# Kernel tuning notes

Measured on AMD Instinct MI355X. Metric: run time of the kernel, lower is better.

## Reference

```python
import jax, jax.numpy as jnp
import numpy as np

NUM_EXPERTS = 8
HIDDEN = 1024
FFN = 2048
TOKENS = 2048


def setup_inputs() -> dict:
    key = jax.random.key(0)
    k_x, k_idx, k_w1, k_w2 = jax.random.split(key, 4)
    scale = 0.02
    x = jax.random.normal(k_x, (TOKENS, HIDDEN), dtype=jnp.float32)
    expert_indices = jax.random.randint(k_idx, (TOKENS,), 0, NUM_EXPERTS, dtype=jnp.int64)
    W1 = jax.random.normal(k_w1, (NUM_EXPERTS, HIDDEN, FFN), dtype=jnp.float32) * scale
    b1 = jnp.zeros((NUM_EXPERTS, FFN), dtype=jnp.float32)
    W2 = jax.random.normal(k_w2, (NUM_EXPERTS, FFN, HIDDEN), dtype=jnp.float32) * scale
    b2 = jnp.zeros((NUM_EXPERTS, HIDDEN), dtype=jnp.float32)
    return {"x": x, "expert_indices": expert_indices, "W1": W1, "b1": b1, "W2": W2, "b2": b2}


def reference(x, expert_indices, W1, b1, W2, b2):
    # Each token routed to one expert's MLP: Linear -> GELU(exact) -> Linear.
    # Dropout is identity in eval mode. Loop is over the small fixed expert set.
    out = jnp.zeros_like(x)
    for e in range(NUM_EXPERTS):
        h = jax.nn.gelu(x @ W1[e] + b1[e], approximate=False)  # [T, FFN]
        y = h @ W2[e] + b2[e]                                   # [T, H]
        mask = (expert_indices == e)[:, None]
        out = out + jnp.where(mask, y, 0.0)
    return out
```

## Files before the change

kernel.cpp:

```cpp
#include <hip/hip_runtime.h>

#define T_TOK 2048
#define HID   1024
#define FFN   2048
#define NEXP  8
#define MAX_SLOTS 40

typedef __attribute__((ext_vector_type(8))) short bf16x8;
typedef __attribute__((ext_vector_type(4))) float f32x4;

__device__ __forceinline__ short f2bf(float f) {
    unsigned u = __builtin_bit_cast(unsigned, f);
    u = (u + 0x7fffu + ((u >> 16) & 1u)) >> 16;
    return (short)u;
}

__device__ __forceinline__ float gelu_exact(float x) {
    return 0.5f * x * (1.0f + erff(x * 0.70710678118654752f));
}

__device__ __forceinline__ void async_cp16(const short* g, short* l) {
    __builtin_amdgcn_global_load_lds(
        (const __attribute__((address_space(1))) unsigned int*)g,
        (__attribute__((address_space(3))) unsigned int*)l, 16, 0, 0);
}

__device__ __forceinline__ void wtrans_body(
        const float* __restrict__ W, short* __restrict__ WT,
        int K, int N, int e, int kblk, int nblk) {
    int tid = threadIdx.x;
    int w = tid >> 6, l = tid & 63;
    int kb = kblk * 32 + w * 8;
    int n4 = nblk * 256 + l * 4;
    const float* src = W + (size_t)e * K * N + (size_t)kb * N + n4;
    float4 v[8];
#pragma unroll
    for (int r = 0; r < 8; r++)
        v[r] = *(const float4*)(src + (size_t)r * N);
    int kpanel = kb >> 6;
    int kc = (kb >> 3) & 7;
    int npanel = n4 >> 7;
    int n_in = n4 & 127;
    int kpanels = K >> 6;
    short* dst = WT + (size_t)e * K * N
               + ((size_t)npanel * kpanels + kpanel) * 8192
               + kc * 1024 + n_in * 8;
#pragma unroll
    for (int j = 0; j < 4; j++) {
        bf16x8 o = {f2bf(((const float*)&v[0])[j]), f2bf(((const float*)&v[1])[j]),
                    f2bf(((const float*)&v[2])[j]), f2bf(((const float*)&v[3])[j]),
                    f2bf(((const float*)&v[4])[j]), f2bf(((const float*)&v[5])[j]),
                    f2bf(((const float*)&v[6])[j]), f2bf(((const float*)&v[7])[j])};
        *(bf16x8*)(dst + j * 8) = o;
    }
}

__global__ __launch_bounds__(256) void wtrans_w1_kernel(
        const float* __restrict__ W1, short* __restrict__ W1T) {
    int e = blockIdx.x >> 8, rem = blockIdx.x & 255;
    wtrans_body(W1, W1T, HID, FFN, e, rem & 31, rem >> 5);
}

__global__ __launch_bounds__(256) void wtrans_w2_kernel(
        const float* __restrict__ W2, short* __restrict__ W2T) {
    int e = blockIdx.x >> 8, rem = blockIdx.x & 255;
    wtrans_body(W2, W2T, FFN, HID, e, rem & 63, rem >> 6);
}

__global__ __launch_bounds__(256) void misc_kernel(
        const float* __restrict__ x, const int* __restrict__ idx,
        const float* __restrict__ b2,
        short* __restrict__ xb, float* __restrict__ out,
        int* __restrict__ offs, int* __restrict__ cnts,
        int* __restrict__ tokl,
        int* __restrict__ slot_e, int* __restrict__ slot_t0) {
    int bx = blockIdx.x;
    int tid = threadIdx.x;
    if (bx < 1024) {
        int i = (bx * 256 + tid) * 8;
        float4 v0 = *(const float4*)(x + i);
        float4 v1 = *(const float4*)(x + i + 4);
        bf16x8 r = {f2bf(v0.x), f2bf(v0.y), f2bf(v0.z), f2bf(v0.w),
                    f2bf(v1.x), f2bf(v1.y), f2bf(v1.z), f2bf(v1.w)};
        *(bf16x8*)(xb + i) = r;
    } else if (bx < 3072) {
        int t = bx - 1024;
        int e = idx[t];
        ((float4*)(out + (size_t)t * HID))[tid] =
            ((const float4*)(b2 + (size_t)e * HID))[tid];
    } else {
        __shared__ int c[NEXP], cur[NEXP], o[NEXP];
        if (tid < NEXP) { c[tid] = 0; cur[tid] = 0; }
        __syncthreads();
        for (int t = tid; t < T_TOK; t += 256) atomicAdd(&c[idx[t]], 1);
        __syncthreads();
        if (tid == 0) {
            int s = 0;
            for (int e = 0; e < NEXP; e++) { o[e] = s; s += c[e]; }
            int ns = 0;
            for (int e = 0; e < NEXP; e++)
                for (int t0 = 0; t0 < c[e]; t0 += 64) {
                    slot_e[ns] = e; slot_t0[ns] = t0; ns++;
                }
            for (; ns < MAX_SLOTS; ns++) slot_e[ns] = -1;
        }
        __syncthreads();
        if (tid < NEXP) { offs[tid] = o[tid]; cnts[tid] = c[tid]; }
        for (int t = tid; t < T_TOK; t += 256) {
            int e = idx[t];
            int p = o[e] + atomicAdd(&cur[e], 1);
            tokl[p] = t;
        }
    }
}

__global__ __launch_bounds__(256) void gemm1_kernel(
        const short* __restrict__ xb, const short* __restrict__ W1T,
        const float* __restrict__ b1,
        const int* __restrict__ offs, const int* __restrict__ cnts,
        const int* __restrict__ tokl,
        const int* __restrict__ slot_e, const int* __restrict__ slot_t0,
        short* __restrict__ hg) {
    int s = blockIdx.y;
    int e = slot_e[s];
    if (e < 0) return;
    int t0 = slot_t0[s], count = cnts[e], off = offs[e];
    int n0 = blockIdx.x * 128;

    __shared__ short As[64 * 64];
    __shared__ short Bs[8 * 128 * 8];
    __shared__ int stok[64];

    int tid = threadIdx.x;
    if (tid < 64) {
        int p = t0 + tid;
        stok[tid] = tokl[off + (p < count ? p : count - 1)];
    }
    __syncthreads();

    int w = tid >> 6, l = tid & 63, l15 = l & 15, quad = l >> 4;
    int wm = (w >> 1) * 32, wn = (w & 1) * 64;

    int m0 = w * 16 + (l >> 3), m1 = m0 + 8;
    int cs = l & 7;
    int c0 = (cs - m0) & 7, c1 = (cs - m1) & 7;
    const short* gA0 = xb + (size_t)stok[m0] * HID + c0 * 8;
    const short* gA1 = xb + (size_t)stok[m1] * HID + c1 * 8;
    short* lA0 = As + w * 1024 + l * 8;
    short* lA1 = lA0 + 512;

    const short* Bpan = W1T + (size_t)e * (FFN * HID)
                      + (size_t)(n0 >> 7) * ((HID >> 6) * 8192);
    int bo0 = (2 * w) * 1024 + l * 8;
    int bo1 = bo0 + 1024;
    int bo2 = bo0 + 512;
    int bo3 = bo1 + 512;

    f32x4 acc[2][4];
#pragma unroll
    for (int i = 0; i < 2; i++)
#pragma unroll
        for (int j = 0; j < 4; j++) acc[i][j] = (f32x4){0.f, 0.f, 0.f, 0.f};

    for (int kt = 0; kt < HID / 64; kt++) {
        const short* bp = Bpan + kt * 8192;
        async_cp16(gA0, lA0);
        async_cp16(gA1, lA1);
        async_cp16(bp + bo0, Bs + bo0);
        async_cp16(bp + bo1, Bs + bo1);
        async_cp16(bp + bo2, Bs + bo2);
        async_cp16(bp + bo3, Bs + bo3);
        gA0 += 64; gA1 += 64;
        __syncthreads();
        bf16x8 a[2][2], b[2][4];
#pragma unroll
        for (int kk = 0; kk < 2; kk++) {
#pragma unroll
            for (int mt = 0; mt < 2; mt++) {
                int m = wm + mt * 16 + l15;
                a[kk][mt] = *(const bf16x8*)&As[m * 64 + (((kk * 4 + quad) + m) & 7) * 8];
            }
#pragma unroll
            for (int nt = 0; nt < 4; nt++) {
                int n = wn + nt * 16 + l15;
                b[kk][nt] = *(const bf16x8*)&Bs[(kk * 4 + quad) * 1024 + n * 8];
            }
        }
#pragma unroll
        for (int kk = 0; kk < 2; kk++)
#pragma unroll
            for (int mt = 0; mt < 2; mt++)
#pragma unroll
                for (int nt = 0; nt < 4; nt++)
                    acc[mt][nt] = __builtin_amdgcn_mfma_f32_16x16x32_bf16(
                        a[kk][mt], b[kk][nt], acc[mt][nt], 0, 0, 0);
        __syncthreads();
    }

    const float* b1e = b1 + e * FFN + n0;
#pragma unroll
    for (int mt = 0; mt < 2; mt++) {
        int rbase = wm + mt * 16 + quad * 4;
#pragma unroll
        for (int nt = 0; nt < 4; nt++) {
            int coln = wn + nt * 16 + l15;
            float bb = b1e[coln];
#pragma unroll
            for (int r = 0; r < 4; r++) {
                int p = t0 + rbase + r;
                if (p < count)
                    hg[(size_t)(off + p) * FFN + n0 + coln] =
                        f2bf(gelu_exact(acc[mt][nt][r] + bb));
            }
        }
    }
}

__global__ __launch_bounds__(256) void gemm2_kernel(
        const short* __restrict__ hg, const short* __restrict__ W2T,
        const int* __restrict__ offs, const int* __restrict__ cnts,
        const int* __restrict__ tokl,
        const int* __restrict__ slot_e, const int* __restrict__ slot_t0,
        float* __restrict__ out) {
    int s = blockIdx.y;
    int e = slot_e[s];
    if (e < 0) return;
    int t0 = slot_t0[s], count = cnts[e], off = offs[e];
    int ks = blockIdx.z;
    int n0 = blockIdx.x * 128;

    __shared__ short As[64 * 64];
    __shared__ short Bs[8 * 128 * 8];

    int tid = threadIdx.x;
    int w = tid >> 6, l = tid & 63, l15 = l & 15, quad = l >> 4;
    int wm = (w >> 1) * 32, wn = (w & 1) * 64;

    int m0 = w * 16 + (l >> 3), m1 = m0 + 8;
    int cs = l & 7;
    int c0 = (cs - m0) & 7, c1 = (cs - m1) & 7;
    int g0 = off + (t0 + m0 < count ? t0 + m0 : count - 1);
    int g1 = off + (t0 + m1 < count ? t0 + m1 : count - 1);
    const short* gA0 = hg + (size_t)g0 * FFN + ks * 1024 + c0 * 8;
    const short* gA1 = hg + (size_t)g1 * FFN + ks * 1024 + c1 * 8;
    short* lA0 = As + w * 1024 + l * 8;
    short* lA1 = lA0 + 512;

    const short* Bpan = W2T + (size_t)e * (FFN * HID)
                      + (size_t)(n0 >> 7) * ((FFN >> 6) * 8192)
                      + (size_t)ks * 16 * 8192;
    int bo0 = (2 * w) * 1024 + l * 8;
    int bo1 = bo0 + 1024;
    int bo2 = bo0 + 512;
    int bo3 = bo1 + 512;

    f32x4 acc[2][4];
#pragma unroll
    for (int i = 0; i < 2; i++)
#pragma unroll
        for (int j = 0; j < 4; j++) acc[i][j] = (f32x4){0.f, 0.f, 0.f, 0.f};

    for (int kt = 0; kt < 16; kt++) {
        const short* bp = Bpan + kt * 8192;
        async_cp16(gA0, lA0);
        async_cp16(gA1, lA1);
        async_cp16(bp + bo0, Bs + bo0);
        async_cp16(bp + bo1, Bs + bo1);
        async_cp16(bp + bo2, Bs + bo2);
        async_cp16(bp + bo3, Bs + bo3);
        gA0 += 64; gA1 += 64;
        __syncthreads();
        bf16x8 a[2][2], b[2][4];
#pragma unroll
        for (int kk = 0; kk < 2; kk++) {
#pragma unroll
            for (int mt = 0; mt < 2; mt++) {
                int m = wm + mt * 16 + l15;
                a[kk][mt] = *(const bf16x8*)&As[m * 64 + (((kk * 4 + quad) + m) & 7) * 8];
            }
#pragma unroll
            for (int nt = 0; nt < 4; nt++) {
                int n = wn + nt * 16 + l15;
                b[kk][nt] = *(const bf16x8*)&Bs[(kk * 4 + quad) * 1024 + n * 8];
            }
        }
#pragma unroll
        for (int kk = 0; kk < 2; kk++)
#pragma unroll
            for (int mt = 0; mt < 2; mt++)
#pragma unroll
                for (int nt = 0; nt < 4; nt++)
                    acc[mt][nt] = __builtin_amdgcn_mfma_f32_16x16x32_bf16(
                        a[kk][mt], b[kk][nt], acc[mt][nt], 0, 0, 0);
        __syncthreads();
    }

#pragma unroll
    for (int mt = 0; mt < 2; mt++) {
        int rbase = wm + mt * 16 + quad * 4;
#pragma unroll
        for (int nt = 0; nt < 4; nt++) {
            int coln = n0 + wn + nt * 16 + l15;
#pragma unroll
            for (int r = 0; r < 4; r++) {
                int p = t0 + rbase + r;
                if (p < count) {
                    int tok = tokl[off + p];
                    atomicAdd(out + (size_t)tok * HID + coln, acc[mt][nt][r]);
                }
            }
        }
    }
}

extern "C" void kernel_launch(void* const* d_in, const int* in_sizes, int n_in,
                              void* d_out, int out_size, void* d_ws, size_t ws_size,
                              hipStream_t stream) {
    const float* x   = (const float*)d_in[0];
    const int*   idx = (const int*)d_in[1];
    const float* W1  = (const float*)d_in[2];
    const float* b1  = (const float*)d_in[3];
    const float* W2  = (const float*)d_in[4];
    const float* b2  = (const float*)d_in[5];
    float* out = (float*)d_out;

    const size_t META = 32768;
    int*   offs    = (int*)d_ws;
    int*   cnts    = offs + 8;
    int*   tokl    = offs + 16;
    int*   slot_e  = offs + 16 + T_TOK;
    int*   slot_t0 = slot_e + MAX_SLOTS;
    char*  base    = (char*)d_ws + META;
    short* xb  = (short*)base;
    short* hg  = (short*)(base + (size_t)T_TOK * HID * 2);
    short* W1T = (short*)(base + (size_t)T_TOK * HID * 2 + (size_t)T_TOK * FFN * 2);
    short* W2T = W1T + (size_t)NEXP * FFN * HID;

    wtrans_w1_kernel<<<2048, 256, 0, stream>>>(W1, W1T);
    wtrans_w2_kernel<<<2048, 256, 0, stream>>>(W2, W2T);
    misc_kernel<<<3073, 256, 0, stream>>>(
        x, idx, b2, xb, out, offs, cnts, tokl, slot_e, slot_t0);

    gemm1_kernel<<<dim3(FFN / 128, MAX_SLOTS), 256, 0, stream>>>(
        xb, W1T, b1, offs, cnts, tokl, slot_e, slot_t0, hg);
    gemm2_kernel<<<dim3(HID / 128, MAX_SLOTS, 2), 256, 0, stream>>>(
        hg, W2T, offs, cnts, tokl, slot_e, slot_t0, out);
}
```

Measured before the change: 236.3 us.

## Triple-buffer LDS tiles with async prefetch in both expert GEMM kernels

```diff
diff --git a/kernel.cpp b/kernel.cpp
--- a/kernel.cpp
+++ b/kernel.cpp
@@ -127,8 +127,8 @@
     int t0 = slot_t0[s], count = cnts[e], off = offs[e];
     int n0 = blockIdx.x * 128;
 
-    __shared__ short As[64 * 64];
-    __shared__ short Bs[8 * 128 * 8];
+    __shared__ short As[3 * 64 * 64];
+    __shared__ short Bs[3 * 8 * 128 * 8];
     __shared__ int stok[64];
 
     int tid = threadIdx.x;
@@ -146,8 +146,7 @@
     int c0 = (cs - m0) & 7, c1 = (cs - m1) & 7;
     const short* gA0 = xb + (size_t)stok[m0] * HID + c0 * 8;
     const short* gA1 = xb + (size_t)stok[m1] * HID + c1 * 8;
-    short* lA0 = As + w * 1024 + l * 8;
-    short* lA1 = lA0 + 512;
+    int aoff = w * 1024 + l * 8;
 
     const short* Bpan = W1T + (size_t)e * (FFN * HID)
                       + (size_t)(n0 >> 7) * ((HID >> 6) * 8192);
@@ -156,34 +155,48 @@
     int bo2 = bo0 + 512;
     int bo3 = bo1 + 512;
 
+    auto stage = [&](int buf, int kt) {
+        const short* bp = Bpan + (size_t)kt * 8192;
+        short* As_b = As + buf * 4096;
+        short* Bs_b = Bs + buf * 8192;
+        async_cp16(gA0 + kt * 64, As_b + aoff);
+        async_cp16(gA1 + kt * 64, As_b + aoff + 512);
+        async_cp16(bp + bo0, Bs_b + bo0);
+        async_cp16(bp + bo1, Bs_b + bo1);
+        async_cp16(bp + bo2, Bs_b + bo2);
+        async_cp16(bp + bo3, Bs_b + bo3);
+    };
+
     f32x4 acc[2][4];
 #pragma unroll
     for (int i = 0; i < 2; i++)
 #pragma unroll
         for (int j = 0; j < 4; j++) acc[i][j] = (f32x4){0.f, 0.f, 0.f, 0.f};
 
-    for (int kt = 0; kt < HID / 64; kt++) {
-        const short* bp = Bpan + kt * 8192;
-        async_cp16(gA0, lA0);
-        async_cp16(gA1, lA1);
-        async_cp16(bp + bo0, Bs + bo0);
-        async_cp16(bp + bo1, Bs + bo1);
-        async_cp16(bp + bo2, Bs + bo2);
-        async_cp16(bp + bo3, Bs + bo3);
-        gA0 += 64; gA1 += 64;
-        __syncthreads();
+    const int KT = HID / 64;
+    stage(0, 0); stage(1, 1); stage(2, 2);
+
+    int buf = 0;
+    for (int kt = 0; kt < KT; kt++) {
+        if (kt + 2 < KT)      asm volatile("s_waitcnt vmcnt(12)" ::: "memory");
+        else if (kt + 1 < KT) asm volatile("s_waitcnt vmcnt(6)" ::: "memory");
+        else                  asm volatile("s_waitcnt vmcnt(0)" ::: "memory");
+        __builtin_amdgcn_s_barrier();
+
+        const short* As_b = As + buf * 4096;
+        const short* Bs_b = Bs + buf * 8192;
         bf16x8 a[2][2], b[2][4];
 #pragma unroll
         for (int kk = 0; kk < 2; kk++) {
 #pragma unroll
             for (int mt = 0; mt < 2; mt++) {
                 int m = wm + mt * 16 + l15;
-                a[kk][mt] = *(const bf16x8*)&As[m * 64 + (((kk * 4 + quad) + m) & 7) * 8];
+                a[kk][mt] = *(const bf16x8*)&As_b[m * 64 + (((kk * 4 + quad) + m) & 7) * 8];
             }
 #pragma unroll
             for (int nt = 0; nt < 4; nt++) {
                 int n = wn + nt * 16 + l15;
-                b[kk][nt] = *(const bf16x8*)&Bs[(kk * 4 + quad) * 1024 + n * 8];
+                b[kk][nt] = *(const bf16x8*)&Bs_b[(kk * 4 + quad) * 1024 + n * 8];
             }
         }
 #pragma unroll
@@ -194,7 +207,11 @@
                 for (int nt = 0; nt < 4; nt++)
                     acc[mt][nt] = __builtin_amdgcn_mfma_f32_16x16x32_bf16(
                         a[kk][mt], b[kk][nt], acc[mt][nt], 0, 0, 0);
-        __syncthreads();
+
+        __builtin_amdgcn_sched_barrier(0);
+        __builtin_amdgcn_s_barrier();
+        if (kt + 3 < KT) stage(buf, kt + 3);
+        buf = buf + 1; if (buf == 3) buf = 0;
     }
 
     const float* b1e = b1 + e * FFN + n0;
@@ -229,8 +246,8 @@
     int ks = blockIdx.z;
     int n0 = blockIdx.x * 128;
 
-    __shared__ short As[64 * 64];
-    __shared__ short Bs[8 * 128 * 8];
+    __shared__ short As[3 * 64 * 64];
+    __shared__ short Bs[3 * 8 * 128 * 8];
 
     int tid = threadIdx.x;
     int w = tid >> 6, l = tid & 63, l15 = l & 15, quad = l >> 4;
@@ -243,8 +260,7 @@
     int g1 = off + (t0 + m1 < count ? t0 + m1 : count - 1);
     const short* gA0 = hg + (size_t)g0 * FFN + ks * 1024 + c0 * 8;
     const short* gA1 = hg + (size_t)g1 * FFN + ks * 1024 + c1 * 8;
-    short* lA0 = As + w * 1024 + l * 8;
-    short* lA1 = lA0 + 512;
+    int aoff = w * 1024 + l * 8;
 
     const short* Bpan = W2T + (size_t)e * (FFN * HID)
                       + (size_t)(n0 >> 7) * ((FFN >> 6) * 8192)
@@ -254,34 +270,48 @@
     int bo2 = bo0 + 512;
     int bo3 = bo1 + 512;
 
+    auto stage = [&](int buf, int kt) {
+        const short* bp = Bpan + (size_t)kt * 8192;
+        short* As_b = As + buf * 4096;
+        short* Bs_b = Bs + buf * 8192;
+        async_cp16(gA0 + kt * 64, As_b + aoff);
+        async_cp16(gA1 + kt * 64, As_b + aoff + 512);
+        async_cp16(bp + bo0, Bs_b + bo0);
+        async_cp16(bp + bo1, Bs_b + bo1);
+        async_cp16(bp + bo2, Bs_b + bo2);
+        async_cp16(bp + bo3, Bs_b + bo3);
+    };
+
     f32x4 acc[2][4];
 #pragma unroll
     for (int i = 0; i < 2; i++)
 #pragma unroll
         for (int j = 0; j < 4; j++) acc[i][j] = (f32x4){0.f, 0.f, 0.f, 0.f};
 
-    for (int kt = 0; kt < 16; kt++) {
-        const short* bp = Bpan + kt * 8192;
-        async_cp16(gA0, lA0);
-        async_cp16(gA1, lA1);
-        async_cp16(bp + bo0, Bs + bo0);
-        async_cp16(bp + bo1, Bs + bo1);
-        async_cp16(bp + bo2, Bs + bo2);
-        async_cp16(bp + bo3, Bs + bo3);
-        gA0 += 64; gA1 += 64;
-        __syncthreads();
+    const int KT = 16;
+    stage(0, 0); stage(1, 1); stage(2, 2);
+
+    int buf = 0;
+    for (int kt = 0; kt < KT; kt++) {
+        if (kt + 2 < KT)      asm volatile("s_waitcnt vmcnt(12)" ::: "memory");
+        else if (kt + 1 < KT) asm volatile("s_waitcnt vmcnt(6)" ::: "memory");
+        else                  asm volatile("s_waitcnt vmcnt(0)" ::: "memory");
+        __builtin_amdgcn_s_barrier();
+
+        const short* As_b = As + buf * 4096;
+        const short* Bs_b = Bs + buf * 8192;
         bf16x8 a[2][2], b[2][4];
 #pragma unroll
         for (int kk = 0; kk < 2; kk++) {
 #pragma unroll
             for (int mt = 0; mt < 2; mt++) {
                 int m = wm + mt * 16 + l15;
-                a[kk][mt] = *(const bf16x8*)&As[m * 64 + (((kk * 4 + quad) + m) & 7) * 8];
+                a[kk][mt] = *(const bf16x8*)&As_b[m * 64 + (((kk * 4 + quad) + m) & 7) * 8];
             }
 #pragma unroll
             for (int nt = 0; nt < 4; nt++) {
                 int n = wn + nt * 16 + l15;
-                b[kk][nt] = *(const bf16x8*)&Bs[(kk * 4 + quad) * 1024 + n * 8];
+                b[kk][nt] = *(const bf16x8*)&Bs_b[(kk * 4 + quad) * 1024 + n * 8];
             }
         }
 #pragma unroll
@@ -292,7 +322,11 @@
                 for (int nt = 0; nt < 4; nt++)
                     acc[mt][nt] = __builtin_amdgcn_mfma_f32_16x16x32_bf16(
                         a[kk][mt], b[kk][nt], acc[mt][nt], 0, 0, 0);
-        __syncthreads();
+
+        __builtin_amdgcn_sched_barrier(0);
+        __builtin_amdgcn_s_barrier();
+        if (kt + 3 < KT) stage(buf, kt + 3);
+        buf = buf + 1; if (buf == 3) buf = 0;
     }
 
 #pragma unroll
```

After: 270.8 us. +14.6%, slower.
